# Kernel tuning notes

Measured on AMD Instinct MI355X. Metric: run time of the kernel, lower is better.

The kernel has to match this reference:

```python
import jax, jax.numpy as jnp
import numpy as np

T = 0.07  # temperature from __init__ default


def setup_inputs() -> dict:
    key = jax.random.key(0)
    ks = jax.random.split(key, 5)
    B, D, H, E = 4096, 2048, 2048, 128
    init = lambda k, shp, fan: jax.random.normal(k, shp, dtype=jnp.float32) * (1.0 / np.sqrt(fan))
    return {
        "input1": jax.random.normal(ks[0], (B, D), dtype=jnp.float32),
        "input2": jax.random.normal(ks[1], (B, D), dtype=jnp.float32),
        "W0": init(ks[2], (D, H), D), "b0": jnp.zeros((H,), jnp.float32),
        "W1": init(ks[3], (H, H), H), "b1": jnp.zeros((H,), jnp.float32),
        "W2": init(ks[4], (H, E), H), "b2": jnp.zeros((E,), jnp.float32),
    }


def _mlp(x, W0, b0, W1, b1, W2, b2):
    # Linear -> ReLU -> Linear -> Linear (ReLU only between hidden layers)
    x = jax.nn.relu(x @ W0 + b0)
    x = x @ W1 + b1
    return x @ W2 + b2


def reference(input1, input2, W0, b0, W1, b1, W2, b2):
    B = input1.shape[0]
    e1 = _mlp(input1, W0, b0, W1, b1, W2, b2)
    e2 = _mlp(input2, W0, b0, W1, b1, W2, b2)
    feats = jnp.stack([e1, e2], axis=1)                       # [B, 2, E]
    feats = feats / jnp.linalg.norm(feats, axis=2, keepdims=True)
    # view(N,2,dim).permute(1,0,2).reshape(2N,dim): view0 rows then view1 rows
    f = jnp.concatenate([feats[:, 0], feats[:, 1]], axis=0)   # [2B, E]
    N2 = 2 * B
    sim = (f @ f.T) / T                                        # [2B, 2B]
    idx = jnp.arange(N2)
    pos = sim[idx, (idx + B) % N2]                             # partner view similarity
    # exclude self-similarity (diagonal) from the logsumexp denominator
    sim = jnp.where(jnp.eye(N2, dtype=bool), jnp.float32(-1e9), sim)
    # CE with positive at index 0 of [pos, negatives] == -pos + logsumexp(non-self)
    loss = jnp.mean(jax.nn.logsumexp(sim, axis=1) - pos)
    return loss
```

## Files before the change

### kernel.cpp

```cpp
#include <hip/hip_runtime.h>
#include <stdint.h>

typedef float f32x4 __attribute__((ext_vector_type(4)));
typedef float f32x16 __attribute__((ext_vector_type(16)));
typedef __bf16 bf16x8 __attribute__((ext_vector_type(8)));
typedef unsigned short u16;
typedef unsigned int u32;

#define INVT 14.285714285714286f
#define L2E  1.4426950408889634f

__device__ __forceinline__ u16 f2bf(float f) {
  u32 u = __float_as_uint(f);
  u32 r = (u + 0x7fffu + ((u >> 16) & 1u)) >> 16;
  return (u16)r;
}
__device__ __forceinline__ float bf2f(u16 h) { return __uint_as_float(((u32)h) << 16); }

__device__ __forceinline__ void g2l16(const void* g, void* l) {
  auto gp = reinterpret_cast<__attribute__((address_space(1))) uint32_t*>(
      reinterpret_cast<uintptr_t>(g));
  auto lp = reinterpret_cast<__attribute__((address_space(3))) uint32_t*>(
      reinterpret_cast<uintptr_t>(l));
  __builtin_amdgcn_global_load_lds(gp, lp, 16, 0, 0);
}


__global__ __launch_bounds__(256) void k_prep(const float* __restrict__ in1,
                                              const float* __restrict__ in2,
                                              u16* __restrict__ Xb,
                                              const float* __restrict__ w0, u16* __restrict__ w0t,
                                              const float* __restrict__ w1, u16* __restrict__ w1t,
                                              const float* __restrict__ w2, u16* __restrict__ w2t) {
  const int bid = blockIdx.x;
  const int tid = threadIdx.x;
  if (bid < 2048) {
    __shared__ u16 tl[64][136];
    const int rb = bid >> 4, cb = bid & 15;
    const int R0 = rb * 64, C0 = cb * 128;
    const float* src = (R0 < 4096 ? in1 : in2);
    const int Rs = (R0 < 4096 ? R0 : R0 - 4096);
    const int r = tid >> 2;
    const int cbase = (tid & 3) * 8;
#pragma unroll
    for (int p = 0; p < 4; ++p) {
      const int c = cbase + p * 32;
      const float* sp = src + (size_t)(Rs + r) * 2048 + C0 + c;
      float4 v0 = *(const float4*)sp;
      float4 v1 = *(const float4*)(sp + 4);
      u16* d = &tl[r][c];
      d[0] = f2bf(v0.x); d[1] = f2bf(v0.y); d[2] = f2bf(v0.z); d[3] = f2bf(v0.w);
      d[4] = f2bf(v1.x); d[5] = f2bf(v1.y); d[6] = f2bf(v1.z); d[7] = f2bf(v1.w);
    }
    __syncthreads();
    const int u = tid >> 4, t16 = tid & 15;
    const int g = u >> 3, s = u & 7;
    const int c0 = t16 >> 3, lmb = (t16 & 7) * 4;
    u16* dst = Xb + (size_t)(cb * 8 + s) * 131072 + (rb * 2 + g) * 512 + t16 * 32;
#pragma unroll
    for (int q = 0; q < 4; ++q)
      *(uint4*)(dst + q * 8) = *(const uint4*)&tl[g * 32 + lmb + q][s * 16 + c0 * 8];
    return;
  }
  if (bid < 6144) {
    const int l = tid & 63, w = tid >> 6;
    const int lm = l & 31, ch = l >> 5;
    const int v = (bid - 2048) * 4 + w;
    const int z = v >> 13, u2 = v & 8191;
    const int s = u2 & 127, g = u2 >> 7;
    const float* Wm = z ? w1 : w0;
    u16* O = z ? w1t : w0t;
    const float* src = Wm + (size_t)(s * 16 + ch * 8) * 2048 + g * 32 + lm;
    float f0 = src[0];
    float f1 = src[2048];
    float f2 = src[2 * 2048];
    float f3 = src[3 * 2048];
    float f4 = src[4 * 2048];
    float f5 = src[5 * 2048];
    float f6 = src[6 * 2048];
    float f7 = src[7 * 2048];
    uint4 o;
    o.x = (u32)f2bf(f0) | ((u32)f2bf(f1) << 16);
    o.y = (u32)f2bf(f2) | ((u32)f2bf(f3) << 16);
    o.z = (u32)f2bf(f4) | ((u32)f2bf(f5) << 16);
    o.w = (u32)f2bf(f6) | ((u32)f2bf(f7) << 16);
    *(uint4*)(O + (size_t)s * 32768 + g * 512 + l * 8) = o;
    return;
  }
  __shared__ float t[64][65];
  const int f = bid - 6144;
  const float* in = w2;
  u16* out = w2t;
  const int C = 128, R = 2048;
  const int r0 = (f >> 1) * 64, c0t = (f & 1) * 64;
#pragma unroll
  for (int p = 0; p < 16; ++p) {
    int idx = p * 256 + tid;
    int r = idx >> 6, c = idx & 63;
    t[r][c] = in[(size_t)(r0 + r) * C + (c0t + c)];
  }
  __syncthreads();
#pragma unroll
  for (int p = 0; p < 16; ++p) {
    int idx = p * 256 + tid;
    int c = idx >> 6, r = idx & 63;
    out[(size_t)(c0t + c) * R + (r0 + r)] = f2bf(t[r][c]);
  }
}

__global__ __launch_bounds__(512, 2) void k_gemm(const u16* __restrict__ A, const u16* __restrict__ Bt,
                                                 const float* __restrict__ bias, u16* __restrict__ C,
                                                 int M, int N, int K, int relu, int blockedC) {
  __shared__ __align__(16) u16 sm[65536];
  const int tid = threadIdx.x;
  const int l = tid & 63, w = tid >> 6;
  const int wm = w >> 2, wn = w & 3;
  const int lm = l & 31, c0 = l >> 5;

  const int bid0 = blockIdx.y * 8 + blockIdx.x;
  const int xcd = bid0 & 7, slot = bid0 >> 3;
  const int bx = (xcd & 1) * 4 + (slot & 3);
  const int by = (xcd >> 1) * 8 + (slot >> 2);
  const int m0 = by * 256, n0 = bx * 256;

  const char* gA = (const char*)A + (size_t)((m0 >> 5) + w) * 1024 + l * 16;
  const char* gB = (const char*)Bt + (size_t)((n0 >> 5) + w) * 1024 + l * 16;
  const size_t slabA = (size_t)M * 32, slabB = (size_t)N * 32;

  auto issue_half = [&](int t, int part, int stg) {
    const int h = part >> 1, isB = part & 1;
    const char* g = isB ? gB : gA;
    const size_t slab = isB ? slabB : slabA;
    const int s0 = t * 4 + h * 2;
    char* lb = (char*)sm + stg * 65536 + isB * 32768 + h * 16384 + w * 1024 + l * 16;
    g2l16(g + (size_t)s0 * slab, lb);
    g2l16(g + (size_t)(s0 + 1) * slab, lb + 8192);
  };

  f32x16 acc[4][2] = {};
  const int NT = K >> 6;

  issue_half(0, 0, 0); issue_half(0, 1, 0); issue_half(0, 2, 0); issue_half(0, 3, 0);
  asm volatile("s_waitcnt vmcnt(4)" ::: "memory");
  asm volatile("s_barrier" ::: "memory");

  for (int kt = 0; kt < NT; ++kt) {
    const u16* bcur = sm + (kt & 1) * 32768;
    const int nstg = (kt & 1) ^ 1;
    const bool pf = (kt + 1) < NT;

#pragma unroll
    for (int k = 0; k < 4; ++k) {
      const u16* As = bcur + (k >> 1) * 8192;
      const u16* Bs = bcur + 16384 + (k >> 1) * 8192;
      const int fb = (k & 1) * 4096 + c0 * 256 + lm * 8;
      bf16x8 a4[4], b2[2];
#pragma unroll
      for (int fm = 0; fm < 4; ++fm)
        a4[fm] = *(const bf16x8*)(As + fb + (wm * 4 + fm) * 512);
#pragma unroll
      for (int fn = 0; fn < 2; ++fn)
        b2[fn] = *(const bf16x8*)(Bs + fb + (wn * 2 + fn) * 512);
      if (pf) issue_half(kt + 1, k, nstg);
      asm volatile("s_barrier" ::: "memory");
      asm volatile("s_waitcnt lgkmcnt(0)" ::: "memory");
      __builtin_amdgcn_sched_barrier(0);
      __builtin_amdgcn_s_setprio(1);
#pragma unroll
      for (int fm = 0; fm < 4; ++fm)
#pragma unroll
        for (int fn = 0; fn < 2; ++fn)
          acc[fm][fn] = __builtin_amdgcn_mfma_f32_32x32x16_bf16(a4[fm], b2[fn],
                                                                acc[fm][fn], 0, 0, 0);
      __builtin_amdgcn_s_setprio(0);
      __builtin_amdgcn_sched_barrier(0);
      if (k & 1) {
        if (pf) asm volatile("s_waitcnt vmcnt(4)" ::: "memory");
        else    asm volatile("s_waitcnt vmcnt(0)" ::: "memory");
      }
      asm volatile("s_barrier" ::: "memory");
    }
  }

  if (blockedC) {
#pragma unroll
    for (int fn = 0; fn < 2; ++fn) {
      const int col = n0 + wn * 64 + lm + fn * 32;
      const float b = bias[col];
      const int sc = col >> 4, cb = (col >> 3) & 1, e = col & 7;
#pragma unroll
      for (int fm = 0; fm < 4; ++fm) {
        const int gg = (m0 >> 5) + wm * 4 + fm;
        u16* base = C + (size_t)sc * ((size_t)M * 16) + gg * 512 + cb * 256 + e;
#pragma unroll
        for (int g = 0; g < 4; ++g)
#pragma unroll
          for (int rr = 0; rr < 4; ++rr) {
            float v = acc[fm][fn][g * 4 + rr] + b;
            if (relu) v = fmaxf(v, 0.0f);
            base[(4 * c0 + g * 8 + rr) * 8] = f2bf(v);
          }
      }
    }
  } else {
    const int colb = n0 + wn * 64 + lm;
    const int rowb = m0 + wm * 128 + 4 * c0;
#pragma unroll
    for (int fn = 0; fn < 2; ++fn) {
      const float b = bias[colb + fn * 32];
#pragma unroll
      for (int fm = 0; fm < 4; ++fm)
#pragma unroll
        for (int g = 0; g < 4; ++g)
#pragma unroll
          for (int rr = 0; rr < 4; ++rr) {
            float v = acc[fm][fn][g * 4 + rr] + b;
            if (relu) v = fmaxf(v, 0.0f);
            C[(size_t)(rowb + fm * 32 + g * 8 + rr) * N + colb + fn * 32] = f2bf(v);
          }
    }
  }
}

__global__ __launch_bounds__(256, 2) void k_gemm_sk(const u16* __restrict__ A, const u16* __restrict__ Bt,
                                                    float* __restrict__ Ep, int K, int Ksplit) {
  __shared__ __align__(16) u16 sm[24576];
  const int tid = threadIdx.x;
  const int l = tid & 63, w = tid >> 6;
  const int wm = w >> 1, wn = w & 1;
  const int m0 = blockIdx.y * 128;
  const int split = blockIdx.x;
  const int k0s = split * Ksplit;

  const int kb = ((l & 3) ^ ((l >> 3) & 3)) * 16;
  const char* gA = (const char*)(A + (size_t)(m0 + w * 16 + (l >> 2)) * K + k0s) + kb;
  const char* gB = (const char*)(Bt + (size_t)(w * 16 + (l >> 2)) * K + k0s) + kb;
  const size_t radv = (size_t)64 * K * 2;

  auto issue = [&](int kcB, int stg) {
    char* base = (char*)sm + stg * 16384;
    char* dA = base + w * 1024 + l * 16;
    char* dB = base + 8192 + w * 1024 + l * 16;
    g2l16(gA + kcB, dA);
    g2l16(gA + radv + kcB, dA + 4096);
    g2l16(gB + kcB, dB);
    g2l16(gB + radv + kcB, dB + 4096);
  };

  const int lm = l & 31;
  const int c0 = l >> 5;
  const int sw = (lm >> 1) & 3;

  f32x16 acc[2][2] = {};

  auto compute = [&](int stg) {
    const u16* As = sm + stg * 8192;
    const u16* Bs = As + 4096;
#pragma unroll
    for (int t = 0; t < 2; ++t) {
      const int cc = (((t << 1) + c0) ^ sw) * 8;
      bf16x8 a2[2], b2[2];
#pragma unroll
      for (int fm = 0; fm < 2; ++fm) a2[fm] = *(const bf16x8*)(As + (wm * 64 + fm * 32 + lm) * 32 + cc);
#pragma unroll
      for (int fn = 0; fn < 2; ++fn) b2[fn] = *(const bf16x8*)(Bs + (wn * 64 + fn * 32 + lm) * 32 + cc);
#pragma unroll
      for (int fm = 0; fm < 2; ++fm)
#pragma unroll
        for (int fn = 0; fn < 2; ++fn)
          acc[fm][fn] = __builtin_amdgcn_mfma_f32_32x32x16_bf16(a2[fm], b2[fn],
                                                                acc[fm][fn], 0, 0, 0);
    }
  };

  const int NK = Ksplit >> 5;
  issue(0, 0);
  issue(64, 1);
  int st = 0;
  for (int kt = 0; kt < NK; ++kt) {
    if (kt + 1 < NK) asm volatile("s_waitcnt vmcnt(4)" ::: "memory");
    else             asm volatile("s_waitcnt vmcnt(0)" ::: "memory");
    asm volatile("s_barrier" ::: "memory");
    if (kt + 2 < NK) {
      int stp = st + 2; if (stp >= 3) stp -= 3;
      issue((kt + 2) * 64, stp);
    }
    compute(st);
    ++st; if (st == 3) st = 0;
  }

  const int colb = wn * 64 + lm;
  const int rowb = m0 + wm * 64 + 4 * c0;
#pragma unroll
  for (int fn = 0; fn < 2; ++fn)
#pragma unroll
    for (int fm = 0; fm < 2; ++fm)
#pragma unroll
      for (int g = 0; g < 4; ++g)
#pragma unroll
        for (int rr = 0; rr < 4; ++rr)
          Ep[((size_t)split * 8192 + rowb + fm * 32 + g * 8 + rr) * 128 + colb + fn * 32] =
              acc[fm][fn][g * 4 + rr];
}

__global__ __launch_bounds__(256) void k_norm(const float* __restrict__ Ep,
                                              const float* __restrict__ b2, u16* __restrict__ F) {
  const int l = threadIdx.x & 63, w = threadIdx.x >> 6;
  const int row = blockIdx.x * 4 + w;
  const float2* base = (const float2*)Ep + (size_t)row * 64 + l;
  float x = 0.f, y = 0.f;
#pragma unroll
  for (int s = 0; s < 4; ++s) {
    float2 t = base[(size_t)s * (8192 * 64)];
    x += t.x; y += t.y;
  }
  x += b2[l * 2]; y += b2[l * 2 + 1];
  float sq = x * x + y * y;
#pragma unroll
  for (int off = 1; off < 64; off <<= 1) sq += __shfl_xor(sq, off);
  const float inv = 1.0f / sqrtf(sq);
  F[(size_t)row * 128 + l * 2] = f2bf(x * inv);
  F[(size_t)row * 128 + l * 2 + 1] = f2bf(y * inv);
}

__global__ __launch_bounds__(256, 2) void k_sim(const u16* __restrict__ F, float* __restrict__ Sp) {
  __shared__ __align__(16) u16 sm[32768];
  const int tid = threadIdx.x;
  const int l = tid & 63, w = tid >> 6;
  const int wm = w >> 1, wn = w & 1;
  const int lm = l & 31, c0 = l >> 5;
  const int r0 = blockIdx.y * 128;
  const int cb0 = blockIdx.x * 1024;

  u16* B0 = sm;
  u16* AB1 = sm + 16384;

  const int srow0 = tid >> 4;
  const int schunk = tid & 15;
  auto stage = [&](const u16* src, u16* dst) {
#pragma unroll
    for (int j = 0; j < 8; ++j) {
      const int row = j * 16 + srow0;
      const int lc = schunk ^ (row & 7);
      g2l16((const char*)(src + (size_t)row * 128) + lc * 16,
            (char*)dst + j * 4096 + tid * 16);
    }
  };

  stage(F + (size_t)r0 * 128, AB1);
  asm volatile("s_waitcnt vmcnt(0)" ::: "memory");
  __syncthreads();

  bf16x8 a[2][8];
#pragma unroll
  for (int fm = 0; fm < 2; ++fm) {
    const int ra = wm * 64 + fm * 32 + lm;
#pragma unroll
    for (int kf = 0; kf < 8; ++kf)
      a[fm][kf] = *(const bf16x8*)(AB1 + ra * 128 + (((kf << 1) + c0) ^ (ra & 7)) * 8);
  }
  asm volatile("s_waitcnt lgkmcnt(0)" ::: "memory");

  stage(F + (size_t)cb0 * 128, B0);

  const float S2 = INVT * L2E;
  const int rB = wn * 64 + lm;
  f32x16 runS[2] = {};

#pragma unroll 1
  for (int p = 0; p < 8; ++p) {
    asm volatile("s_waitcnt vmcnt(0)" ::: "memory");
    asm volatile("s_barrier" ::: "memory");
    if (p < 7) stage(F + (size_t)(cb0 + (p + 1) * 128) * 128, (p & 1) ? B0 : AB1);
    const u16* Bs = (p & 1) ? AB1 : B0;

    f32x16 acc[2][2] = {};
#pragma unroll
    for (int kf = 0; kf < 8; ++kf) {
      const int kc = (kf << 1) + c0;
      bf16x8 b0v = *(const bf16x8*)(Bs + rB * 128 + (kc ^ (rB & 7)) * 8);
      bf16x8 b1v = *(const bf16x8*)(Bs + (rB + 32) * 128 + (kc ^ ((rB + 32) & 7)) * 8);
      acc[0][0] = __builtin_amdgcn_mfma_f32_32x32x16_bf16(a[0][kf], b0v, acc[0][0], 0, 0, 0);
      acc[0][1] = __builtin_amdgcn_mfma_f32_32x32x16_bf16(a[0][kf], b1v, acc[0][1], 0, 0, 0);
      acc[1][0] = __builtin_amdgcn_mfma_f32_32x32x16_bf16(a[1][kf], b0v, acc[1][0], 0, 0, 0);
      acc[1][1] = __builtin_amdgcn_mfma_f32_32x32x16_bf16(a[1][kf], b1v, acc[1][1], 0, 0, 0);
    }

    const int cp = cb0 + p * 128;
    if (cp == r0) {
#pragma unroll
      for (int fm = 0; fm < 2; ++fm)
#pragma unroll
        for (int fn = 0; fn < 2; ++fn) {
          const int rcol = wn * 64 + fn * 32 + lm;
#pragma unroll
          for (int r = 0; r < 16; ++r) {
            const int rrow = wm * 64 + fm * 32 + (r & 3) + 8 * (r >> 2) + 4 * c0;
            float e = exp2f(fmaf(acc[fm][fn][r], S2, -S2));
            if (rrow == rcol) e = 0.f;
            runS[fm][r] += e;
          }
        }
    } else {
#pragma unroll
      for (int fm = 0; fm < 2; ++fm)
#pragma unroll
        for (int fn = 0; fn < 2; ++fn)
#pragma unroll
          for (int r = 0; r < 16; ++r)
            runS[fm][r] += exp2f(fmaf(acc[fm][fn][r], S2, -S2));
    }
  }

#pragma unroll
  for (int fm = 0; fm < 2; ++fm)
#pragma unroll
    for (int r = 0; r < 16; ++r) {
      float s = runS[fm][r];
      s += __shfl_xor(s, 1);
      s += __shfl_xor(s, 2);
      s += __shfl_xor(s, 4);
      s += __shfl_xor(s, 8);
      s += __shfl_xor(s, 16);
      runS[fm][r] = s;
    }

  __syncthreads();
  float* red = (float*)sm;
  if (wn == 0) {
    if (lm == 0) {
#pragma unroll
      for (int fm = 0; fm < 2; ++fm)
#pragma unroll
        for (int r = 0; r < 16; ++r)
          red[wm * 64 + fm * 32 + (r & 3) + 8 * (r >> 2) + 4 * c0] = runS[fm][r];
    }
  }
  __syncthreads();
  if (wn == 1 && lm == 0) {
#pragma unroll
    for (int fm = 0; fm < 2; ++fm)
#pragma unroll
      for (int r = 0; r < 16; ++r) {
        const int rr = wm * 64 + fm * 32 + (r & 3) + 8 * (r >> 2) + 4 * c0;
        Sp[(size_t)blockIdx.x * 8192 + r0 + rr] = red[rr] + runS[fm][r];
      }
  }
}

__global__ __launch_bounds__(256) void k_combine(const float* __restrict__ Sp,
                                                 const u16* __restrict__ F,
                                                 float* __restrict__ out) {
  const int r = blockIdx.x * 256 + threadIdx.x;
  float S = 0.f;
#pragma unroll
  for (int c = 0; c < 8; ++c) S += Sp[c * 8192 + r];
  const float lse = INVT + logf(S);
  const int par = (r + 4096) & 8191;
  const bf16x8* a = (const bf16x8*)(F + (size_t)r * 128);
  const bf16x8* b = (const bf16x8*)(F + (size_t)par * 128);
  float dot = 0.f;
#pragma unroll
  for (int k = 0; k < 16; ++k) {
    bf16x8 va = a[k], vb = b[k];
#pragma unroll
    for (int j = 0; j < 8; ++j) dot = fmaf((float)va[j], (float)vb[j], dot);
  }
  float contrib = lse - dot * INVT;
#pragma unroll
  for (int off = 1; off < 64; off <<= 1) contrib += __shfl_xor(contrib, off);
  if ((threadIdx.x & 63) == 0) atomicAdd(out, contrib * (1.0f / 8192.0f));
}

extern "C" void kernel_launch(void* const* d_in, const int* in_sizes, int n_in,
                              void* d_out, int out_size, void* d_ws, size_t ws_size,
                              hipStream_t stream) {
  const float* input1 = (const float*)d_in[0];
  const float* input2 = (const float*)d_in[1];
  const float* W0 = (const float*)d_in[2];
  const float* b0 = (const float*)d_in[3];
  const float* W1 = (const float*)d_in[4];
  const float* b1 = (const float*)d_in[5];
  const float* W2 = (const float*)d_in[6];
  const float* b2 = (const float*)d_in[7];
  float* out = (float*)d_out;
  char* ws = (char*)d_ws;

  u16* Xb = (u16*)(ws + 0);
  u16* H1 = (u16*)(ws + 33554432);
  u16* W0T = (u16*)(ws + 67108864);
  u16* W1T = (u16*)(ws + 75497472);
  float* Ep = (float*)(ws + 67108864);
  u16* W2T = (u16*)(ws + 83886080);
  float* Sp = (float*)(ws + 83886080);
  u16* Ff = (u16*)(ws + 84410368);
  u16* H2 = Xb;

  hipMemsetAsync(d_out, 0, sizeof(float), stream);
  k_prep<<<6208, 256, 0, stream>>>(input1, input2, Xb, W0, W0T, W1, W1T, W2, W2T);
  k_gemm<<<dim3(8, 32), 512, 0, stream>>>(Xb, W0T, b0, H1, 8192, 2048, 2048, 1, 1);
  k_gemm<<<dim3(8, 32), 512, 0, stream>>>(H1, W1T, b1, H2, 8192, 2048, 2048, 0, 0);
  k_gemm_sk<<<dim3(4, 64), 256, 0, stream>>>(H2, W2T, Ep, 2048, 512);
  k_norm<<<2048, 256, 0, stream>>>(Ep, b2, Ff);
  k_sim<<<dim3(8, 64), 256, 0, stream>>>(Ff, Sp);
  k_combine<<<32, 256, 0, stream>>>(Sp, Ff, out);
}
```

Baseline: 325.6 us.

## Double-buffer LDS fragment registers and drop per-substep barriers in GEMM mainloop

```diff
diff --git a/kernel.cpp b/kernel.cpp
--- a/kernel.cpp
+++ b/kernel.cpp
@@ -137,49 +137,68 @@
     g2l16(g + (size_t)(s0 + 1) * slab, lb + 8192);
   };
 
+  const int fbase = c0 * 256 + lm * 8;
+  bf16x8 aX[4], bX[2], aY[4], bY[2];
+
+  auto ldfrag = [&](int buf, int k, bf16x8* a, bf16x8* b) {
+    const u16* base = sm + buf * 32768;
+    const u16* As = base + (k >> 1) * 8192;
+    const u16* Bs = base + 16384 + (k >> 1) * 8192;
+    const int fb = (k & 1) * 4096 + fbase;
+#pragma unroll
+    for (int fm = 0; fm < 4; ++fm)
+      a[fm] = *(const bf16x8*)(As + fb + (wm * 4 + fm) * 512);
+#pragma unroll
+    for (int fn = 0; fn < 2; ++fn)
+      b[fn] = *(const bf16x8*)(Bs + fb + (wn * 2 + fn) * 512);
+  };
+
   f32x16 acc[4][2] = {};
+  auto mfma8 = [&](bf16x8* a, bf16x8* b) {
+    __builtin_amdgcn_s_setprio(1);
+#pragma unroll
+    for (int fm = 0; fm < 4; ++fm)
+#pragma unroll
+      for (int fn = 0; fn < 2; ++fn)
+        acc[fm][fn] = __builtin_amdgcn_mfma_f32_32x32x16_bf16(a[fm], b[fn],
+                                                              acc[fm][fn], 0, 0, 0);
+    __builtin_amdgcn_s_setprio(0);
+  };
+
   const int NT = K >> 6;
 
   issue_half(0, 0, 0); issue_half(0, 1, 0); issue_half(0, 2, 0); issue_half(0, 3, 0);
-  asm volatile("s_waitcnt vmcnt(4)" ::: "memory");
+  asm volatile("s_waitcnt vmcnt(0)" ::: "memory");
   asm volatile("s_barrier" ::: "memory");
+  ldfrag(0, 0, aX, bX);
 
   for (int kt = 0; kt < NT; ++kt) {
-    const u16* bcur = sm + (kt & 1) * 32768;
-    const int nstg = (kt & 1) ^ 1;
+    const int buf = kt & 1, nbuf = buf ^ 1;
     const bool pf = (kt + 1) < NT;
 
-#pragma unroll
-    for (int k = 0; k < 4; ++k) {
-      const u16* As = bcur + (k >> 1) * 8192;
-      const u16* Bs = bcur + 16384 + (k >> 1) * 8192;
-      const int fb = (k & 1) * 4096 + c0 * 256 + lm * 8;
-      bf16x8 a4[4], b2[2];
-#pragma unroll
-      for (int fm = 0; fm < 4; ++fm)
-        a4[fm] = *(const bf16x8*)(As + fb + (wm * 4 + fm) * 512);
-#pragma unroll
-      for (int fn = 0; fn < 2; ++fn)
-        b2[fn] = *(const bf16x8*)(Bs + fb + (wn * 2 + fn) * 512);
-      if (pf) issue_half(kt + 1, k, nstg);
-      asm volatile("s_barrier" ::: "memory");
-      asm volatile("s_waitcnt lgkmcnt(0)" ::: "memory");
-      __builtin_amdgcn_sched_barrier(0);
-      __builtin_amdgcn_s_setprio(1);
-#pragma unroll
-      for (int fm = 0; fm < 4; ++fm)
-#pragma unroll
-        for (int fn = 0; fn < 2; ++fn)
-          acc[fm][fn] = __builtin_amdgcn_mfma_f32_32x32x16_bf16(a4[fm], b2[fn],
-                                                                acc[fm][fn], 0, 0, 0);
-      __builtin_amdgcn_s_setprio(0);
-      __builtin_amdgcn_sched_barrier(0);
-      if (k & 1) {
-        if (pf) asm volatile("s_waitcnt vmcnt(4)" ::: "memory");
-        else    asm volatile("s_waitcnt vmcnt(0)" ::: "memory");
-      }
-      asm volatile("s_barrier" ::: "memory");
-    }
+    if (pf) { issue_half(kt + 1, 0, nbuf); issue_half(kt + 1, 1, nbuf); }
+    ldfrag(buf, 1, aY, bY);
+    asm volatile("s_waitcnt lgkmcnt(6)" ::: "memory");
+    __builtin_amdgcn_sched_barrier(0);
+    mfma8(aX, bX);
+
+    if (pf) { issue_half(kt + 1, 2, nbuf); issue_half(kt + 1, 3, nbuf); }
+    ldfrag(buf, 2, aX, bX);
+    asm volatile("s_waitcnt lgkmcnt(6)" ::: "memory");
+    __builtin_amdgcn_sched_barrier(0);
+    mfma8(aY, bY);
+
+    ldfrag(buf, 3, aY, bY);
+    asm volatile("s_waitcnt lgkmcnt(6)" ::: "memory");
+    __builtin_amdgcn_sched_barrier(0);
+    mfma8(aX, bX);
+
+    asm volatile("s_waitcnt lgkmcnt(0)" ::: "memory");
+    __builtin_amdgcn_sched_barrier(0);
+    mfma8(aY, bY);
+    asm volatile("s_waitcnt vmcnt(0)" ::: "memory");
+    asm volatile("s_barrier" ::: "memory");
+    if (pf) ldfrag(nbuf, 0, aX, bX);
   }
 
   if (blockedC) {
```

Result: no change. 331.1 us (+1.7%).

## Restructure main GEMM to 128x256 tiles with 3-stage LDS pipeline

Applied to the files above, without the earlier changes.

```diff
diff --git a/kernel.cpp b/kernel.cpp
--- a/kernel.cpp
+++ b/kernel.cpp
@@ -108,89 +108,94 @@
   }
 }
 
-__global__ __launch_bounds__(512, 2) void k_gemm(const u16* __restrict__ A, const u16* __restrict__ Bt,
+__global__ __launch_bounds__(256, 2) void k_gemm(const u16* __restrict__ A, const u16* __restrict__ Bt,
                                                  const float* __restrict__ bias, u16* __restrict__ C,
                                                  int M, int N, int K, int relu, int blockedC) {
-  __shared__ __align__(16) u16 sm[65536];
+  __shared__ __align__(16) u16 sm[36864];
   const int tid = threadIdx.x;
   const int l = tid & 63, w = tid >> 6;
-  const int wm = w >> 2, wn = w & 3;
   const int lm = l & 31, c0 = l >> 5;
 
   const int bid0 = blockIdx.y * 8 + blockIdx.x;
   const int xcd = bid0 & 7, slot = bid0 >> 3;
-  const int bx = (xcd & 1) * 4 + (slot & 3);
-  const int by = (xcd >> 1) * 8 + (slot >> 2);
-  const int m0 = by * 256, n0 = bx * 256;
-
-  const char* gA = (const char*)A + (size_t)((m0 >> 5) + w) * 1024 + l * 16;
-  const char* gB = (const char*)Bt + (size_t)((n0 >> 5) + w) * 1024 + l * 16;
+  const int by = xcd * 8 + (slot >> 3), bx = slot & 7;
+  const int m0 = by * 128, n0 = bx * 256;
+
+  const char* gA = (const char*)A + (size_t)(m0 >> 5) * 1024 + l * 16;
+  const char* gB = (const char*)Bt + (size_t)(n0 >> 5) * 1024 + l * 16;
   const size_t slabA = (size_t)M * 32, slabB = (size_t)N * 32;
 
-  auto issue_half = [&](int t, int part, int stg) {
-    const int h = part >> 1, isB = part & 1;
-    const char* g = isB ? gB : gA;
-    const size_t slab = isB ? slabB : slabA;
-    const int s0 = t * 4 + h * 2;
-    char* lb = (char*)sm + stg * 65536 + isB * 32768 + h * 16384 + w * 1024 + l * 16;
-    g2l16(g + (size_t)s0 * slab, lb);
-    g2l16(g + (size_t)(s0 + 1) * slab, lb + 8192);
+  auto stage_tile = [&](int t, int stg) {
+    char* base = (char*)sm + stg * 24576;
+#pragma unroll
+    for (int i = 0; i < 6; ++i) {
+      const int u = w * 6 + i;
+      const int isB = u >= 8;
+      const int v = isB ? u - 8 : u;
+      const int k16 = isB ? (v >> 3) : (v >> 2);
+      const int rg = isB ? (v & 7) : (v & 3);
+      const char* g = (isB ? gB : gA) + (size_t)(t * 2 + k16) * (isB ? slabB : slabA) + rg * 1024;
+      char* lb = base + (isB ? 8192 + (k16 * 8 + rg) * 1024 : (k16 * 4 + rg) * 1024) + l * 16;
+      g2l16(g, lb);
+    }
   };
 
+  auto ldfrag = [&](int stg, int k16, bf16x8* a, bf16x8* b) {
+    const u16* As = sm + stg * 12288 + k16 * 2048;
+    const u16* Bs = sm + stg * 12288 + 4096 + (k16 * 8 + w * 2) * 512;
+#pragma unroll
+    for (int fm = 0; fm < 4; ++fm) a[fm] = *(const bf16x8*)(As + fm * 512 + l * 8);
+#pragma unroll
+    for (int fn = 0; fn < 2; ++fn) b[fn] = *(const bf16x8*)(Bs + fn * 512 + l * 8);
+  };
+
   f32x16 acc[4][2] = {};
-  const int NT = K >> 6;
-
-  issue_half(0, 0, 0); issue_half(0, 1, 0); issue_half(0, 2, 0); issue_half(0, 3, 0);
-  asm volatile("s_waitcnt vmcnt(4)" ::: "memory");
+  auto mfma8 = [&](bf16x8* a, bf16x8* b) {
+#pragma unroll
+    for (int fm = 0; fm < 4; ++fm)
+#pragma unroll
+      for (int fn = 0; fn < 2; ++fn)
+        acc[fm][fn] = __builtin_amdgcn_mfma_f32_32x32x16_bf16(a[fm], b[fn],
+                                                              acc[fm][fn], 0, 0, 0);
+  };
+
+  const int NT = K >> 5;
+
+  stage_tile(0, 0);
+  stage_tile(1, 1);
+  asm volatile("s_waitcnt vmcnt(6)" ::: "memory");
   asm volatile("s_barrier" ::: "memory");
 
-  for (int kt = 0; kt < NT; ++kt) {
-    const u16* bcur = sm + (kt & 1) * 32768;
-    const int nstg = (kt & 1) ^ 1;
-    const bool pf = (kt + 1) < NT;
-
-#pragma unroll
-    for (int k = 0; k < 4; ++k) {
-      const u16* As = bcur + (k >> 1) * 8192;
-      const u16* Bs = bcur + 16384 + (k >> 1) * 8192;
-      const int fb = (k & 1) * 4096 + c0 * 256 + lm * 8;
-      bf16x8 a4[4], b2[2];
-#pragma unroll
-      for (int fm = 0; fm < 4; ++fm)
-        a4[fm] = *(const bf16x8*)(As + fb + (wm * 4 + fm) * 512);
-#pragma unroll
-      for (int fn = 0; fn < 2; ++fn)
-        b2[fn] = *(const bf16x8*)(Bs + fb + (wn * 2 + fn) * 512);
-      if (pf) issue_half(kt + 1, k, nstg);
+  int stg = 0;
+  for (int t = 0; t < NT; ++t) {
+    int stg2 = stg + 2; if (stg2 >= 3) stg2 -= 3;
+    if (t + 2 < NT) stage_tile(t + 2, stg2);
+
+    bf16x8 a0[4], b0[2], a1[4], b1[2];
+    ldfrag(stg, 0, a0, b0);
+    ldfrag(stg, 1, a1, b1);
+    __builtin_amdgcn_s_setprio(1);
+    mfma8(a0, b0);
+    mfma8(a1, b1);
+    __builtin_amdgcn_s_setprio(0);
+
+    if (t + 1 < NT) {
+      if (t + 2 < NT) asm volatile("s_waitcnt vmcnt(6) lgkmcnt(0)" ::: "memory");
+      else            asm volatile("s_waitcnt vmcnt(0) lgkmcnt(0)" ::: "memory");
       asm volatile("s_barrier" ::: "memory");
-      asm volatile("s_waitcnt lgkmcnt(0)" ::: "memory");
-      __builtin_amdgcn_sched_barrier(0);
-      __builtin_amdgcn_s_setprio(1);
-#pragma unroll
-      for (int fm = 0; fm < 4; ++fm)
-#pragma unroll
-        for (int fn = 0; fn < 2; ++fn)
-          acc[fm][fn] = __builtin_amdgcn_mfma_f32_32x32x16_bf16(a4[fm], b2[fn],
-                                                                acc[fm][fn], 0, 0, 0);
-      __builtin_amdgcn_s_setprio(0);
-      __builtin_amdgcn_sched_barrier(0);
-      if (k & 1) {
-        if (pf) asm volatile("s_waitcnt vmcnt(4)" ::: "memory");
-        else    asm volatile("s_waitcnt vmcnt(0)" ::: "memory");
-      }
-      asm volatile("s_barrier" ::: "memory");
-    }
+    }
+    ++stg; if (stg == 3) stg = 0;
   }
 
   if (blockedC) {
 #pragma unroll
     for (int fn = 0; fn < 2; ++fn) {
-      const int col = n0 + wn * 64 + lm + fn * 32;
+      const int col = n0 + w * 64 + lm + fn * 32;
       const float b = bias[col];
       const int sc = col >> 4, cb = (col >> 3) & 1, e = col & 7;
 #pragma unroll
       for (int fm = 0; fm < 4; ++fm) {
-        const int gg = (m0 >> 5) + wm * 4 + fm;
+        const int gg = (m0 >> 5) + fm;
         u16* base = C + (size_t)sc * ((size_t)M * 16) + gg * 512 + cb * 256 + e;
 #pragma unroll
         for (int g = 0; g < 4; ++g)
@@ -203,8 +208,8 @@
       }
     }
   } else {
-    const int colb = n0 + wn * 64 + lm;
-    const int rowb = m0 + wm * 128 + 4 * c0;
+    const int colb = n0 + w * 64 + lm;
+    const int rowb = m0 + 4 * c0;
 #pragma unroll
     for (int fn = 0; fn < 2; ++fn) {
       const float b = bias[colb + fn * 32];
@@ -498,8 +503,8 @@
 
   hipMemsetAsync(d_out, 0, sizeof(float), stream);
   k_prep<<<6208, 256, 0, stream>>>(input1, input2, Xb, W0, W0T, W1, W1T, W2, W2T);
-  k_gemm<<<dim3(8, 32), 512, 0, stream>>>(Xb, W0T, b0, H1, 8192, 2048, 2048, 1, 1);
-  k_gemm<<<dim3(8, 32), 512, 0, stream>>>(H1, W1T, b1, H2, 8192, 2048, 2048, 0, 0);
+  k_gemm<<<dim3(8, 64), 256, 0, stream>>>(Xb, W0T, b0, H1, 8192, 2048, 2048, 1, 1);
+  k_gemm<<<dim3(8, 64), 256, 0, stream>>>(H1, W1T, b1, H2, 8192, 2048, 2048, 0, 0);
   k_gemm_sk<<<dim3(4, 64), 256, 0, stream>>>(H2, W2T, Ep, 2048, 512);
   k_norm<<<2048, 256, 0, stream>>>(Ep, b2, Ff);
   k_sim<<<dim3(8, 64), 256, 0, stream>>>(Ff, Sp);
```

Measured after the change: 347.8 us. +6.8%, slower.
